# Optimization experiments

Hardware: AMD Instinct MI355X
Metric: run time of the kernel (lower is better)

The kernel has to match this reference:

```python
import jax, jax.numpy as jnp
import numpy as np

N, D_IN, D_ATTN = 8192, 48, 8


def setup_inputs() -> dict:
    key = jax.random.key(0)
    ks = jax.random.split(key, 9)
    s = 1.0 / np.sqrt(D_IN)
    return {
        "x": jax.random.normal(ks[0], (N, D_IN), jnp.float32),
        "Kw": jax.random.normal(ks[1], (D_IN, D_ATTN), jnp.float32) * s,
        "Kb": jax.random.normal(ks[2], (D_ATTN,), jnp.float32) * s,
        "Qw": jax.random.normal(ks[3], (D_IN, D_ATTN), jnp.float32) * s,
        "Qb": jax.random.normal(ks[4], (D_ATTN,), jnp.float32) * s,
        "Vw": jax.random.normal(ks[5], (D_IN, D_ATTN), jnp.float32) * s,
        "Vb": jax.random.normal(ks[6], (D_ATTN,), jnp.float32) * s,
        "Zw": jax.random.normal(ks[7], (D_ATTN, D_IN), jnp.float32) * (1.0 / np.sqrt(D_ATTN)),
        "Zb": jax.random.normal(ks[8], (D_IN,), jnp.float32) * (1.0 / np.sqrt(D_ATTN)),
    }


def reference(x, Kw, Kb, Qw, Qb, Vw, Vb, Zw, Zb):
    # Tiny QKV projections: [N,48] -> [N,8]
    Xk = x @ Kw + Kb
    Xq = x @ Qw + Qb
    Xv = x @ Vw + Vb
    # Attention over the batch/row dimension: [N,8]@[8,N] -> [N,N]
    scale = jnp.sqrt(jnp.asarray(D_ATTN, jnp.float32))
    AM = jax.nn.softmax(Xk @ Xq.T / scale, axis=1)  # torch F.softmax 2D default dim=1
    Z = AM @ Xv                                      # [N,8]
    return x + (Z @ Zw + Zb)                         # residual + output proj [N,48]
```

## Files before the change

kernel.cpp:

```cpp
#include <hip/hip_runtime.h>
#include <hip/hip_fp16.h>


#define QV_OFF   32768
#define BMAX_OFF 98304
#define PART_OFF 98560

typedef _Float16 hv2 __attribute__((ext_vector_type(2)));
union HVU { unsigned u; hv2 v; };

static __device__ __forceinline__ unsigned pku(float a, float b) {
    auto t = __builtin_amdgcn_cvt_pkrtz(a, b);
    union { decltype(t) x; unsigned u; } c; c.x = t; return c.u;
}
static __device__ __forceinline__ float loF(unsigned u) { HVU t; t.u = u; return (float)t.v.x; }
static __device__ __forceinline__ float hiF(unsigned u) { HVU t; t.u = u; return (float)t.v.y; }
static __device__ __forceinline__ unsigned pkfma(unsigned a, unsigned b, unsigned c) {
    unsigned d;
    asm("v_pk_fma_f16 %0, %1, %2, %3" : "=v"(d) : "v"(a), "v"(b), "v"(c));
    return d;
}
static __device__ __forceinline__ unsigned dupL(unsigned u) {
    const unsigned lo = u & 0xFFFFu; return lo | (lo << 16);
}
static __device__ __forceinline__ unsigned dupH(unsigned u) {
    const unsigned hi = u >> 16; return hi | (hi << 16);
}

__global__ __launch_bounds__(256) void proj_kernel(
    const float* __restrict__ x,
    const float* __restrict__ Kw, const float* __restrict__ Kb,
    const float* __restrict__ Qw, const float* __restrict__ Qb,
    const float* __restrict__ Vw, const float* __restrict__ Vb,
    unsigned* __restrict__ Xksf16, unsigned* __restrict__ QV,
    float* __restrict__ bmax)
{
    __shared__ float xs[32 * 49];
    __shared__ float wAll[3 * 388];
    __shared__ float bs[24];
    __shared__ float outv[32][25];
    const int tid = threadIdx.x;
    const int r0 = blockIdx.x * 32;

    for (int i = tid; i < 1536; i += 256) {
        int r = i / 48, c = i - r * 48;
        xs[r * 49 + c] = x[r0 * 48 + i];
    }
    for (int i = tid; i < 384; i += 256) {
        wAll[i]       = Kw[i];
        wAll[388 + i] = Qw[i];
        wAll[776 + i] = Vw[i];
    }
    if (tid < 8)       bs[tid] = Kb[tid];
    else if (tid < 16) bs[tid] = Qb[tid - 8];
    else if (tid < 24) bs[tid] = Vb[tid - 16];
    __syncthreads();

    const int rl = tid >> 3;
    const int g  = tid & 7;
    const int c0 = 3 * g;
    const float* xr = &xs[rl * 49];
    const float* w0 = &wAll[((c0 + 0) >> 3) * 388 + ((c0 + 0) & 7)];
    const float* w1 = &wAll[((c0 + 1) >> 3) * 388 + ((c0 + 1) & 7)];
    const float* w2 = &wAll[((c0 + 2) >> 3) * 388 + ((c0 + 2) & 7)];
    float a0 = bs[c0], a1 = bs[c0 + 1], a2 = bs[c0 + 2];
    #pragma unroll
    for (int k = 0; k < 48; k++) {
        const float xv = xr[k];
        a0 = fmaf(xv, w0[k * 8], a0);
        a1 = fmaf(xv, w1[k * 8], a1);
        a2 = fmaf(xv, w2[k * 8], a2);
    }
    outv[rl][c0] = a0; outv[rl][c0 + 1] = a1; outv[rl][c0 + 2] = a2;
    __syncthreads();

    {
        const int p = tid >> 4;
        const int c = (tid >> 1) & 7;
        const int m = tid & 1;
        const int col = (m ? 16 : 8) + c;
        QV[(blockIdx.x * 16 + p) * 16 + m * 8 + c] =
            pku(outv[2 * p][col], outv[2 * p + 1][col]);
    }
    const float kscale = 0.51008732149f;
    if (tid < 32) {
        uint4 o;
        o.x = pku(outv[tid][0] * kscale, outv[tid][1] * kscale);
        o.y = pku(outv[tid][2] * kscale, outv[tid][3] * kscale);
        o.z = pku(outv[tid][4] * kscale, outv[tid][5] * kscale);
        o.w = pku(outv[tid][6] * kscale, outv[tid][7] * kscale);
        ((uint4*)Xksf16)[r0 + tid] = o;
    }
    if (tid >= 192 && tid < 224) {
        const int r = tid - 192;
        float n2 = 0.f;
        #pragma unroll
        for (int c = 0; c < 8; c++) n2 = fmaf(outv[r][8 + c], outv[r][8 + c], n2);
        #pragma unroll
        for (int off = 16; off > 0; off >>= 1)
            n2 = fmaxf(n2, __shfl_xor(n2, off, 64));
        if (r == 0) bmax[blockIdx.x] = n2;
    }
}

__global__ __launch_bounds__(256) void attn_kernel(
    const unsigned* __restrict__ Xksf16, const unsigned* __restrict__ QV,
    const float* __restrict__ bmax,
    float* __restrict__ part, int ppw)
{
    __shared__ uint4 sh4[2304];
    uint4* slab = sh4;
    float* redf = (float*)sh4;

    const int tid  = threadIdx.x;
    const int lane = tid & 63;
    const int wv   = tid >> 6;
    const int rgrp  = blockIdx.x & 31;
    const int chunk = blockIdx.x >> 5;

    float m = fmaxf(fmaxf(bmax[lane], bmax[64 + lane]),
                    fmaxf(bmax[128 + lane], bmax[192 + lane]));
    #pragma unroll
    for (int off = 32; off > 0; off >>= 1)
        m = fmaxf(m, __shfl_xor(m, off, 64));
    const float qmax2 = m;

    unsigned kd[4][8];
    unsigned sinit2[4], l2[4], acc[4][8];
    const unsigned ONE2 = 0x3C003C00u;
    #pragma unroll
    for (int i = 0; i < 4; ++i) {
        const uint4 kv = ((const uint4*)Xksf16)[rgrp * 256 + i * 64 + lane];
        kd[i][0] = dupL(kv.x); kd[i][1] = dupH(kv.x);
        kd[i][2] = dupL(kv.y); kd[i][3] = dupH(kv.y);
        kd[i][4] = dupL(kv.z); kd[i][5] = dupH(kv.z);
        kd[i][6] = dupL(kv.w); kd[i][7] = dupH(kv.w);
        float kn2 = 0.f;
        #pragma unroll
        for (int c = 0; c < 8; c++) {
            const float kf = loF(kd[i][c]);
            kn2 = fmaf(kf, kf, kn2);
        }
        const float sinit = -sqrtf(kn2 * qmax2);
        sinit2[i] = pku(sinit, sinit);
        l2[i] = 0u;
        #pragma unroll
        for (int c = 0; c < 8; c++) acc[i][c] = 0u;
    }

    const uint4* QV4 = (const uint4*)QV;
    const int nt = ppw >> 5;

    for (int t = 0; t < nt; ++t) {
        for (int i = tid; i < 512; i += 256) {
            const int w = i >> 7;
            const int j = i & 127;
            slab[i] = QV4[(size_t)((((chunk * 4 + w) * ppw + (t << 5)) << 2) + j)];
        }
        __syncthreads();

        const uint4* sw = &slab[wv << 7];
        #pragma unroll 1
        for (int p = 0; p < 32; ++p) {
            const uint4 qp0 = sw[p * 4 + 0];
            const uint4 qp1 = sw[p * 4 + 1];
            const uint4 vp0 = sw[p * 4 + 2];
            const uint4 vp1 = sw[p * 4 + 3];
            #pragma unroll
            for (int i = 0; i < 4; ++i) {
                unsigned s2 = sinit2[i];
                s2 = pkfma(kd[i][0], qp0.x, s2);
                s2 = pkfma(kd[i][1], qp0.y, s2);
                s2 = pkfma(kd[i][2], qp0.z, s2);
                s2 = pkfma(kd[i][3], qp0.w, s2);
                s2 = pkfma(kd[i][4], qp1.x, s2);
                s2 = pkfma(kd[i][5], qp1.y, s2);
                s2 = pkfma(kd[i][6], qp1.z, s2);
                s2 = pkfma(kd[i][7], qp1.w, s2);
                const float pa = __builtin_amdgcn_exp2f(loF(s2));
                const float pb = __builtin_amdgcn_exp2f(hiF(s2));
                const unsigned ph = pku(pa, pb);
                l2[i] = pkfma(ph, ONE2, l2[i]);
                acc[i][0] = pkfma(ph, vp0.x, acc[i][0]);
                acc[i][1] = pkfma(ph, vp0.y, acc[i][1]);
                acc[i][2] = pkfma(ph, vp0.z, acc[i][2]);
                acc[i][3] = pkfma(ph, vp0.w, acc[i][3]);
                acc[i][4] = pkfma(ph, vp1.x, acc[i][4]);
                acc[i][5] = pkfma(ph, vp1.y, acc[i][5]);
                acc[i][6] = pkfma(ph, vp1.z, acc[i][6]);
                acc[i][7] = pkfma(ph, vp1.w, acc[i][7]);
            }
        }
        __syncthreads();
    }

    #pragma unroll
    for (int i = 0; i < 4; ++i) {
        const int r = i * 64 + lane;
        #pragma unroll
        for (int c = 0; c < 8; c++)
            redf[(wv * 256 + r) * 9 + c] = loF(acc[i][c]) + hiF(acc[i][c]);
        redf[(wv * 256 + r) * 9 + 8] = loF(l2[i]) + hiF(l2[i]);
    }
    __syncthreads();
    for (int e = tid; e < 2304; e += 256) {
        const int r = e / 9, c = e - r * 9;
        const float s = redf[(0 * 256 + r) * 9 + c] + redf[(1 * 256 + r) * 9 + c]
                      + redf[(2 * 256 + r) * 9 + c] + redf[(3 * 256 + r) * 9 + c];
        part[((size_t)chunk * 8192 + rgrp * 256 + r) * 9 + c] = s;
    }
}

__global__ __launch_bounds__(256) void finish_kernel(
    const float* __restrict__ x,
    const float* __restrict__ Zw, const float* __restrict__ Zb,
    const float* __restrict__ part, float* __restrict__ out, int nch)
{
    __shared__ float Zs[32 * 9];
    __shared__ float Zl[32];
    __shared__ float zw_s[384];
    __shared__ float zb_s[48];
    const int tid = threadIdx.x;
    const int r0 = blockIdx.x * 32;

    for (int i = tid; i < 384; i += 256) zw_s[i] = Zw[i];
    if (tid < 48) zb_s[tid] = Zb[tid];

    {
        const int r = tid >> 3, c = tid & 7;
        float a = 0.f, l = 0.f;
        #pragma unroll 4
        for (int ch = 0; ch < nch; ch++) {
            const float* p = part + ((size_t)ch * 8192 + r0 + r) * 9;
            a += p[c];
            if (c == 0) l += p[8];
        }
        if (c == 0) Zl[r] = l;
        __syncthreads();
        Zs[r * 9 + c] = a * (1.0f / Zl[r]);
    }
    __syncthreads();

    for (int e = tid; e < 32 * 48; e += 256) {
        const int r = e / 48, c = e - r * 48;
        float o = x[r0 * 48 + e] + zb_s[c];
        #pragma unroll
        for (int k = 0; k < 8; k++) o = fmaf(Zs[r * 9 + k], zw_s[k * 48 + c], o);
        out[r0 * 48 + e] = o;
    }
}

extern "C" void kernel_launch(void* const* d_in, const int* in_sizes, int n_in,
                              void* d_out, int out_size, void* d_ws, size_t ws_size,
                              hipStream_t stream) {
    const float* x  = (const float*)d_in[0];
    const float* Kw = (const float*)d_in[1];
    const float* Kb = (const float*)d_in[2];
    const float* Qw = (const float*)d_in[3];
    const float* Qb = (const float*)d_in[4];
    const float* Vw = (const float*)d_in[5];
    const float* Vb = (const float*)d_in[6];
    const float* Zw = (const float*)d_in[7];
    const float* Zb = (const float*)d_in[8];
    float* out = (float*)d_out;

    float* ws = (float*)d_ws;
    unsigned* Xksf16 = (unsigned*)ws;
    unsigned* QV     = (unsigned*)(ws + QV_OFF);
    float* bmax      = ws + BMAX_OFF;
    float* part      = ws + PART_OFF;

    int nch = 32;
    const size_t avail = ws_size / 4;
    while (nch > 1 && (size_t)PART_OFF + (size_t)nch * 8192 * 9 > avail) nch >>= 1;
    const int ppw = 1024 / nch;

    proj_kernel<<<256, 256, 0, stream>>>(x, Kw, Kb, Qw, Qb, Vw, Vb,
                                         Xksf16, QV, bmax);
    attn_kernel<<<32 * nch, 256, 0, stream>>>(Xksf16, QV, bmax, part, ppw);
    finish_kernel<<<256, 256, 0, stream>>>(x, Zw, Zb, part, out, nch);
}
```

Measured before the change: 118.6 us.

## Switch attention inner loop from packed fp16 to fp32 FMA with fp32 Q

Replaces the packed-half v_pk_fma_f16 attention inner loop with scalar fp32 FMAs. Q is now stored as fp32 and V as fp16 in a new per-row 12-word record layout, and each wave processes two key rows per iteration. This removes the half-precision accumulation and the pack/unpack conversions. In exchange it roughly doubles the ALU instruction count per score, since packed math did two lanes per instruction, and it raises the staging memory per tile.

After: 125.2 us. 1.06x slower.

```diff
diff --git a/kernel.cpp b/kernel.cpp
--- a/kernel.cpp
+++ b/kernel.cpp
@@ -2,9 +2,9 @@
 #include <hip/hip_fp16.h>
 
 
-#define QV_OFF   32768
-#define BMAX_OFF 98304
-#define PART_OFF 98560
+#define QVJ_OFF  32768
+#define BMAX_OFF 131072
+#define PART_OFF 131328
 
 typedef _Float16 hv2 __attribute__((ext_vector_type(2)));
 union HVU { unsigned u; hv2 v; };
@@ -15,24 +15,13 @@
 }
 static __device__ __forceinline__ float loF(unsigned u) { HVU t; t.u = u; return (float)t.v.x; }
 static __device__ __forceinline__ float hiF(unsigned u) { HVU t; t.u = u; return (float)t.v.y; }
-static __device__ __forceinline__ unsigned pkfma(unsigned a, unsigned b, unsigned c) {
-    unsigned d;
-    asm("v_pk_fma_f16 %0, %1, %2, %3" : "=v"(d) : "v"(a), "v"(b), "v"(c));
-    return d;
-}
-static __device__ __forceinline__ unsigned dupL(unsigned u) {
-    const unsigned lo = u & 0xFFFFu; return lo | (lo << 16);
-}
-static __device__ __forceinline__ unsigned dupH(unsigned u) {
-    const unsigned hi = u >> 16; return hi | (hi << 16);
-}
 
 __global__ __launch_bounds__(256) void proj_kernel(
     const float* __restrict__ x,
     const float* __restrict__ Kw, const float* __restrict__ Kb,
     const float* __restrict__ Qw, const float* __restrict__ Qb,
     const float* __restrict__ Vw, const float* __restrict__ Vb,
-    unsigned* __restrict__ Xksf16, unsigned* __restrict__ QV,
+    unsigned* __restrict__ Xksf16, unsigned* __restrict__ QVJ,
     float* __restrict__ bmax)
 {
     __shared__ float xs[32 * 49];
@@ -74,13 +63,16 @@
     outv[rl][c0] = a0; outv[rl][c0 + 1] = a1; outv[rl][c0 + 2] = a2;
     __syncthreads();
 
-    {
-        const int p = tid >> 4;
-        const int c = (tid >> 1) & 7;
-        const int m = tid & 1;
-        const int col = (m ? 16 : 8) + c;
-        QV[(blockIdx.x * 16 + p) * 16 + m * 8 + c] =
-            pku(outv[2 * p][col], outv[2 * p + 1][col]);
+    for (int i = tid; i < 384; i += 256) {
+        const int r = i / 12, f = i - r * 12;
+        unsigned val;
+        if (f < 8) {
+            val = __float_as_uint(outv[r][8 + f]);
+        } else {
+            const int pp = f - 8;
+            val = pku(outv[r][16 + 2 * pp], outv[r][16 + 2 * pp + 1]);
+        }
+        QVJ[((size_t)blockIdx.x * 32 + r) * 12 + f] = val;
     }
     const float kscale = 0.51008732149f;
     if (tid < 32) {
@@ -104,13 +96,14 @@
 }
 
 __global__ __launch_bounds__(256) void attn_kernel(
-    const unsigned* __restrict__ Xksf16, const unsigned* __restrict__ QV,
+    const unsigned* __restrict__ Xksf16, const unsigned* __restrict__ QVJ,
     const float* __restrict__ bmax,
-    float* __restrict__ part, int ppw)
+    float* __restrict__ part, int jpw)
 {
-    __shared__ uint4 sh4[2304];
-    uint4* slab = sh4;
-    float* redf = (float*)sh4;
+    __shared__ float shf[4 * 256 * 9];
+    uint4*  slab4 = (uint4*)shf;
+    float4* slabf = (float4*)shf;
+    float*  redf  = shf;
 
     const int tid  = threadIdx.x;
     const int lane = tid & 63;
@@ -125,70 +118,79 @@
         m = fmaxf(m, __shfl_xor(m, off, 64));
     const float qmax2 = m;
 
-    unsigned kd[4][8];
-    unsigned sinit2[4], l2[4], acc[4][8];
-    const unsigned ONE2 = 0x3C003C00u;
+    float kf[4][8];
+    float sinit[4], l[4], acc[4][8];
     #pragma unroll
     for (int i = 0; i < 4; ++i) {
         const uint4 kv = ((const uint4*)Xksf16)[rgrp * 256 + i * 64 + lane];
-        kd[i][0] = dupL(kv.x); kd[i][1] = dupH(kv.x);
-        kd[i][2] = dupL(kv.y); kd[i][3] = dupH(kv.y);
-        kd[i][4] = dupL(kv.z); kd[i][5] = dupH(kv.z);
-        kd[i][6] = dupL(kv.w); kd[i][7] = dupH(kv.w);
+        kf[i][0] = loF(kv.x); kf[i][1] = hiF(kv.x);
+        kf[i][2] = loF(kv.y); kf[i][3] = hiF(kv.y);
+        kf[i][4] = loF(kv.z); kf[i][5] = hiF(kv.z);
+        kf[i][6] = loF(kv.w); kf[i][7] = hiF(kv.w);
         float kn2 = 0.f;
         #pragma unroll
-        for (int c = 0; c < 8; c++) {
-            const float kf = loF(kd[i][c]);
-            kn2 = fmaf(kf, kf, kn2);
-        }
-        const float sinit = -sqrtf(kn2 * qmax2);
-        sinit2[i] = pku(sinit, sinit);
-        l2[i] = 0u;
-        #pragma unroll
-        for (int c = 0; c < 8; c++) acc[i][c] = 0u;
-    }
-
-    const uint4* QV4 = (const uint4*)QV;
-    const int nt = ppw >> 5;
+        for (int c = 0; c < 8; c++) kn2 = fmaf(kf[i][c], kf[i][c], kn2);
+        sinit[i] = -sqrtf(kn2 * qmax2);
+        l[i] = 0.f;
+        #pragma unroll
+        for (int c = 0; c < 8; c++) acc[i][c] = 0.f;
+    }
+
+    const uint4* QVJ4 = (const uint4*)QVJ;
+    const int nt = jpw >> 6;
 
     for (int t = 0; t < nt; ++t) {
-        for (int i = tid; i < 512; i += 256) {
-            const int w = i >> 7;
-            const int j = i & 127;
-            slab[i] = QV4[(size_t)((((chunk * 4 + w) * ppw + (t << 5)) << 2) + j)];
+        for (int i = tid; i < 768; i += 256) {
+            const int w = i / 192, rec = i - w * 192;
+            slab4[i] = QVJ4[((size_t)(chunk * 4 + w) * jpw + t * 64) * 3 + rec];
         }
         __syncthreads();
 
-        const uint4* sw = &slab[wv << 7];
+        const int wbase = wv * 192;
         #pragma unroll 1
-        for (int p = 0; p < 32; ++p) {
-            const uint4 qp0 = sw[p * 4 + 0];
-            const uint4 qp1 = sw[p * 4 + 1];
-            const uint4 vp0 = sw[p * 4 + 2];
-            const uint4 vp1 = sw[p * 4 + 3];
+        for (int jj = 0; jj < 32; ++jj) {
+            const int b = wbase + jj * 6;
+            const float4 qa0 = slabf[b + 0];
+            const float4 qa1 = slabf[b + 1];
+            const uint4  va  = slab4[b + 2];
+            const float4 qb0 = slabf[b + 3];
+            const float4 qb1 = slabf[b + 4];
+            const uint4  vb  = slab4[b + 5];
+            const float vA0 = loF(va.x), vA1 = hiF(va.x), vA2 = loF(va.y), vA3 = hiF(va.y);
+            const float vA4 = loF(va.z), vA5 = hiF(va.z), vA6 = loF(va.w), vA7 = hiF(va.w);
+            const float vB0 = loF(vb.x), vB1 = hiF(vb.x), vB2 = loF(vb.y), vB3 = hiF(vb.y);
+            const float vB4 = loF(vb.z), vB5 = hiF(vb.z), vB6 = loF(vb.w), vB7 = hiF(vb.w);
             #pragma unroll
             for (int i = 0; i < 4; ++i) {
-                unsigned s2 = sinit2[i];
-                s2 = pkfma(kd[i][0], qp0.x, s2);
-                s2 = pkfma(kd[i][1], qp0.y, s2);
-                s2 = pkfma(kd[i][2], qp0.z, s2);
-                s2 = pkfma(kd[i][3], qp0.w, s2);
-                s2 = pkfma(kd[i][4], qp1.x, s2);
-                s2 = pkfma(kd[i][5], qp1.y, s2);
-                s2 = pkfma(kd[i][6], qp1.z, s2);
-                s2 = pkfma(kd[i][7], qp1.w, s2);
-                const float pa = __builtin_amdgcn_exp2f(loF(s2));
-                const float pb = __builtin_amdgcn_exp2f(hiF(s2));
-                const unsigned ph = pku(pa, pb);
-                l2[i] = pkfma(ph, ONE2, l2[i]);
-                acc[i][0] = pkfma(ph, vp0.x, acc[i][0]);
-                acc[i][1] = pkfma(ph, vp0.y, acc[i][1]);
-                acc[i][2] = pkfma(ph, vp0.z, acc[i][2]);
-                acc[i][3] = pkfma(ph, vp0.w, acc[i][3]);
-                acc[i][4] = pkfma(ph, vp1.x, acc[i][4]);
-                acc[i][5] = pkfma(ph, vp1.y, acc[i][5]);
-                acc[i][6] = pkfma(ph, vp1.z, acc[i][6]);
-                acc[i][7] = pkfma(ph, vp1.w, acc[i][7]);
+                float sA = sinit[i];
+                sA = fmaf(kf[i][0], qa0.x, sA);
+                sA = fmaf(kf[i][1], qa0.y, sA);
+                sA = fmaf(kf[i][2], qa0.z, sA);
+                sA = fmaf(kf[i][3], qa0.w, sA);
+                sA = fmaf(kf[i][4], qa1.x, sA);
+                sA = fmaf(kf[i][5], qa1.y, sA);
+                sA = fmaf(kf[i][6], qa1.z, sA);
+                sA = fmaf(kf[i][7], qa1.w, sA);
+                float sB = sinit[i];
+                sB = fmaf(kf[i][0], qb0.x, sB);
+                sB = fmaf(kf[i][1], qb0.y, sB);
+                sB = fmaf(kf[i][2], qb0.z, sB);
+                sB = fmaf(kf[i][3], qb0.w, sB);
+                sB = fmaf(kf[i][4], qb1.x, sB);
+                sB = fmaf(kf[i][5], qb1.y, sB);
+                sB = fmaf(kf[i][6], qb1.z, sB);
+                sB = fmaf(kf[i][7], qb1.w, sB);
+                const float pA = __builtin_amdgcn_exp2f(sA);
+                const float pB = __builtin_amdgcn_exp2f(sB);
+                l[i] += pA + pB;
+                acc[i][0] = fmaf(pA, vA0, fmaf(pB, vB0, acc[i][0]));
+                acc[i][1] = fmaf(pA, vA1, fmaf(pB, vB1, acc[i][1]));
+                acc[i][2] = fmaf(pA, vA2, fmaf(pB, vB2, acc[i][2]));
+                acc[i][3] = fmaf(pA, vA3, fmaf(pB, vB3, acc[i][3]));
+                acc[i][4] = fmaf(pA, vA4, fmaf(pB, vB4, acc[i][4]));
+                acc[i][5] = fmaf(pA, vA5, fmaf(pB, vB5, acc[i][5]));
+                acc[i][6] = fmaf(pA, vA6, fmaf(pB, vB6, acc[i][6]));
+                acc[i][7] = fmaf(pA, vA7, fmaf(pB, vB7, acc[i][7]));
             }
         }
         __syncthreads();
@@ -199,8 +201,8 @@
         const int r = i * 64 + lane;
         #pragma unroll
         for (int c = 0; c < 8; c++)
-            redf[(wv * 256 + r) * 9 + c] = loF(acc[i][c]) + hiF(acc[i][c]);
-        redf[(wv * 256 + r) * 9 + 8] = loF(l2[i]) + hiF(l2[i]);
+            redf[(wv * 256 + r) * 9 + c] = acc[i][c];
+        redf[(wv * 256 + r) * 9 + 8] = l[i];
     }
     __syncthreads();
     for (int e = tid; e < 2304; e += 256) {
@@ -266,17 +268,17 @@
 
     float* ws = (float*)d_ws;
     unsigned* Xksf16 = (unsigned*)ws;
-    unsigned* QV     = (unsigned*)(ws + QV_OFF);
+    unsigned* QVJ    = (unsigned*)(ws + QVJ_OFF);
     float* bmax      = ws + BMAX_OFF;
     float* part      = ws + PART_OFF;
 
     int nch = 32;
     const size_t avail = ws_size / 4;
     while (nch > 1 && (size_t)PART_OFF + (size_t)nch * 8192 * 9 > avail) nch >>= 1;
-    const int ppw = 1024 / nch;
+    const int jpw = 2048 / nch;
 
     proj_kernel<<<256, 256, 0, stream>>>(x, Kw, Kb, Qw, Qb, Vw, Vb,
-                                         Xksf16, QV, bmax);
-    attn_kernel<<<32 * nch, 256, 0, stream>>>(Xksf16, QV, bmax, part, ppw);
+                                         Xksf16, QVJ, bmax);
+    attn_kernel<<<32 * nch, 256, 0, stream>>>(Xksf16, QVJ, bmax, part, jpw);
     finish_kernel<<<256, 256, 0, stream>>>(x, Zw, Zb, part, out, nch);
 }
```
